# Kernel tuning notes

Hardware: AMD Instinct MI355X
Metric: run time of the kernel (lower is better)

The kernel has to match this reference:

```python
import jax, jax.numpy as jnp
import numpy as np

CUTOFF_RADIUS = 5.0
ETA = 0.5
ZETA = 1.0
LAMBDA = 1.0


def setup_inputs() -> dict:
    key = jax.random.key(0)
    k1, k2 = jax.random.split(key)
    B, N = 16, 96
    distance_vectors = jax.random.normal(k1, (B, N, N, 3), dtype=jnp.float32)
    # positive distances in (0, 1): within cutoff, no exact zeros off-diagonal
    distances = jax.random.uniform(k2, (B, N, N), dtype=jnp.float32)
    return {"distance_vectors": distance_vectors, "distances": distances}


def reference(distance_vectors, distances):
    # cosines[b,i,j,k] = <r_ij, r_jk> / (d_ij * d_jk)
    dot_products = jnp.einsum('bijd,bjkd->bijk', distance_vectors, distance_vectors)
    magnitudes = jnp.einsum('bij,bjk->bijk', distances, distances)
    cosines = dot_products / magnitudes

    cosine_term = (1.0 + LAMBDA * cosines) ** ZETA
    cosine_term = jnp.nan_to_num(cosine_term, nan=0.0, posinf=0.0, neginf=0.0)

    # exponent[b,i,j,k] = d_ij^2 + d_ik^2 + d_jk^2
    d2 = distances ** 2
    exponent = d2[..., :, :, None] + d2[..., :, None, :] + d2[..., None, :, :]
    exponential_term = jnp.exp(-ETA * exponent)

    # smooth cutoff radial function
    radials = jnp.tanh(1.0 - distances / CUTOFF_RADIUS) ** 3
    radials = jnp.where(distances <= CUTOFF_RADIUS, radials, jnp.zeros_like(distances))
    radial_term = (radials[..., :, :, None]
                   * radials[..., :, None, :]
                   * radials[..., None, :, :])

    coefficient = 2.0 ** (1.0 - ZETA)
    return coefficient * (cosine_term * exponential_term * radial_term).sum(axis=(-1, -2))
```

## Files before the change

kernel.cpp:

```cpp
#include <hip/hip_runtime.h>
#include <hip/hip_bf16.h>


#define B 16
#define N 96
#define KP 128
#define TI 4
#define P2_THREADS 128

__global__ void g4_prep(const float* __restrict__ dv,
                        const float* __restrict__ dist,
                        float4* __restrict__ W) {
    int idx = blockIdx.x * blockDim.x + threadIdx.x;
    if (idx >= B * N * KP) return;
    int k   = idx & (KP - 1);
    int row = idx >> 7;
    float4 w = make_float4(0.f, 0.f, 0.f, 0.f);
    if (k < N) {
        int src = row * N + k;
        float d = dist[src];
        float r = tanhf(1.0f - d * 0.2f);
        float R = r * r * r;
        float f = expf(-0.5f * d * d) * R;
        float q = f / d;
        w.x = f;
        w.y = dv[src * 3 + 0] * q;
        w.z = dv[src * 3 + 1] * q;
        w.w = dv[src * 3 + 2] * q;
    }
    W[idx] = w;
}

__global__ __launch_bounds__(P2_THREADS)
void g4_contract(const float4* __restrict__ W, float* __restrict__ out) {
    const int b  = blockIdx.x / (N / TI);
    const int i0 = (blockIdx.x % (N / TI)) * TI;
    const int t  = threadIdx.x;

    __shared__ float4 rowI[TI][N];

    const float4* Wb = W + (size_t)b * N * KP;

    for (int e = t; e < TI * N; e += P2_THREADS) {
        int ii = e / N, j = e % N;
        rowI[ii][j] = Wb[(i0 + ii) * KP + j];
    }

    float fik[TI];
#pragma unroll
    for (int ii = 0; ii < TI; ++ii)
        fik[ii] = Wb[(i0 + ii) * KP + t].x;

    __syncthreads();

    float acc[TI] = {0.f, 0.f, 0.f, 0.f};
#pragma unroll 4
    for (int j = 0; j < N; ++j) {
        float4 wj = Wb[j * KP + t];
#pragma unroll
        for (int ii = 0; ii < TI; ++ii) {
            float4 ri = rowI[ii][j];
            float inner = ri.x * wj.x + ri.y * wj.y + ri.z * wj.z + ri.w * wj.w;
            acc[ii] = fmaf(fik[ii], inner, acc[ii]);
        }
    }

    __shared__ float red[TI][2];
#pragma unroll
    for (int ii = 0; ii < TI; ++ii) {
        float v = acc[ii];
        for (int off = 32; off > 0; off >>= 1)
            v += __shfl_down(v, off);
        if ((t & 63) == 0) red[ii][t >> 6] = v;
    }
    __syncthreads();
    if (t < TI) {
        out[b * N + i0 + t] = red[t][0] + red[t][1];
    }
}

extern "C" void kernel_launch(void* const* d_in, const int* in_sizes, int n_in,
                              void* d_out, int out_size, void* d_ws, size_t ws_size,
                              hipStream_t stream) {
    const float* dv   = (const float*)d_in[0];
    const float* dist = (const float*)d_in[1];
    float*  out = (float*)d_out;
    float4* W   = (float4*)d_ws;

    {
        int total = B * N * KP;
        int thr = 256;
        int blk = (total + thr - 1) / thr;
        g4_prep<<<blk, thr, 0, stream>>>(dv, dist, W);
    }
    {
        int blk = B * (N / TI);
        g4_contract<<<blk, P2_THREADS, 0, stream>>>(W, out);
    }
}
```

Measured before the change: 77.60 us.

## Split contraction over j into chunks with atomic accumulation

The contraction kernel now splits the j loop into four chunks, each handled by its own block, which raises the grid from 384 to 1536 blocks and improves occupancy across the GPU's many CUs. Partial sums are combined with atomicAdd into the output, which the prep kernel now zeroes. The prep kernel also replaces tanhf with an exp-based formula. Atomic accumulation makes the summation order nondeterministic, and each block repeats the fik loads.

```diff
diff --git a/kernel.cpp b/kernel.cpp
--- a/kernel.cpp
+++ b/kernel.cpp
@@ -6,12 +6,16 @@
 #define N 96
 #define KP 128
 #define TI 4
+#define JS 4
+#define JC (N / JS)
 #define P2_THREADS 128
 
 __global__ void g4_prep(const float* __restrict__ dv,
                         const float* __restrict__ dist,
-                        float4* __restrict__ W) {
+                        float4* __restrict__ W,
+                        float* __restrict__ out) {
     int idx = blockIdx.x * blockDim.x + threadIdx.x;
+    if (idx < B * N) out[idx] = 0.f;
     if (idx >= B * N * KP) return;
     int k   = idx & (KP - 1);
     int row = idx >> 7;
@@ -19,10 +23,10 @@
     if (k < N) {
         int src = row * N + k;
         float d = dist[src];
-        float r = tanhf(1.0f - d * 0.2f);
-        float R = r * r * r;
-        float f = expf(-0.5f * d * d) * R;
-        float q = f / d;
+        float e2 = expf(-2.0f * (1.0f - d * 0.2f));
+        float r  = (1.0f - e2) / (1.0f + e2);
+        float f  = expf(-0.5f * d * d) * r * r * r;
+        float q  = f / d;
         w.x = f;
         w.y = dv[src * 3 + 0] * q;
         w.z = dv[src * 3 + 1] * q;
@@ -33,17 +37,21 @@
 
 __global__ __launch_bounds__(P2_THREADS)
 void g4_contract(const float4* __restrict__ W, float* __restrict__ out) {
-    const int b  = blockIdx.x / (N / TI);
-    const int i0 = (blockIdx.x % (N / TI)) * TI;
-    const int t  = threadIdx.x;
+    const int bi   = blockIdx.x;
+    const int js   = bi % JS;
+    const int rest = bi / JS;
+    const int b    = rest / (N / TI);
+    const int i0   = (rest % (N / TI)) * TI;
+    const int j0   = js * JC;
+    const int t    = threadIdx.x;
 
-    __shared__ float4 rowI[TI][N];
+    __shared__ float4 rowI[TI][JC];
 
     const float4* Wb = W + (size_t)b * N * KP;
 
-    for (int e = t; e < TI * N; e += P2_THREADS) {
-        int ii = e / N, j = e % N;
-        rowI[ii][j] = Wb[(i0 + ii) * KP + j];
+    for (int e = t; e < TI * JC; e += P2_THREADS) {
+        int ii = e / JC, jj = e % JC;
+        rowI[ii][jj] = Wb[(i0 + ii) * KP + j0 + jj];
     }
 
     float fik[TI];
@@ -55,11 +63,11 @@
 
     float acc[TI] = {0.f, 0.f, 0.f, 0.f};
 #pragma unroll 4
-    for (int j = 0; j < N; ++j) {
-        float4 wj = Wb[j * KP + t];
+    for (int jj = 0; jj < JC; ++jj) {
+        float4 wj = Wb[(j0 + jj) * KP + t];
 #pragma unroll
         for (int ii = 0; ii < TI; ++ii) {
-            float4 ri = rowI[ii][j];
+            float4 ri = rowI[ii][jj];
             float inner = ri.x * wj.x + ri.y * wj.y + ri.z * wj.z + ri.w * wj.w;
             acc[ii] = fmaf(fik[ii], inner, acc[ii]);
         }
@@ -69,14 +77,14 @@
 #pragma unroll
     for (int ii = 0; ii < TI; ++ii) {
         float v = acc[ii];
+#pragma unroll
         for (int off = 32; off > 0; off >>= 1)
             v += __shfl_down(v, off);
         if ((t & 63) == 0) red[ii][t >> 6] = v;
     }
     __syncthreads();
-    if (t < TI) {
-        out[b * N + i0 + t] = red[t][0] + red[t][1];
-    }
+    if (t < TI)
+        atomicAdd(&out[b * N + i0 + t], red[t][0] + red[t][1]);
 }
 
 extern "C" void kernel_launch(void* const* d_in, const int* in_sizes, int n_in,
@@ -91,10 +99,10 @@
         int total = B * N * KP;
         int thr = 256;
         int blk = (total + thr - 1) / thr;
-        g4_prep<<<blk, thr, 0, stream>>>(dv, dist, W);
+        g4_prep<<<blk, thr, 0, stream>>>(dv, dist, W, out);
     }
     {
-        int blk = B * (N / TI);
+        int blk = B * (N / TI) * JS;
         g4_contract<<<blk, P2_THREADS, 0, stream>>>(W, out);
     }
 }
```

New measurement: 68.64 us. 11.6% less time.
